# Performance work log

Measured on AMD Instinct MI355X. Metric: run time of the kernel, lower is better.

Reference implementation:

```python
import jax, jax.numpy as jnp
import numpy as np

B, L, D = 2, 1024, 2048
E, K = 8, 2
H, HS = 1408, 2816


def setup_inputs() -> dict:
    key = jax.random.key(0)
    ks = jax.random.split(key, 9)
    s = 0.02  # param init scale
    return {
        "x": jax.random.normal(ks[0], (B, L, D), dtype=jnp.float32),
        "gate_w": jax.random.normal(ks[1], (E, D), dtype=jnp.float32) * s,
        "w_gate": jax.random.normal(ks[2], (E, D, H), dtype=jnp.float32) * s,
        "w_up": jax.random.normal(ks[3], (E, D, H), dtype=jnp.float32) * s,
        "w_down": jax.random.normal(ks[4], (E, H, D), dtype=jnp.float32) * s,
        "shgate_w": jax.random.normal(ks[5], (D,), dtype=jnp.float32) * s,
        "shw_gate": jax.random.normal(ks[6], (D, HS), dtype=jnp.float32) * s,
        "shw_up": jax.random.normal(ks[7], (D, HS), dtype=jnp.float32) * s,
        "shw_down": jax.random.normal(ks[8], (HS, D), dtype=jnp.float32) * s,
    }


def reference(x, gate_w, w_gate, w_up, w_down, shgate_w, shw_gate, shw_up, shw_down):
    b, l, d = x.shape
    xf = x.reshape(-1, d)  # [T, D]

    # --- router: softmax over expert logits, top-k, renormalize ---
    logits = jnp.einsum("td,ed->te", xf.astype(jnp.float32), gate_w)
    probs = jax.nn.softmax(logits.astype(jnp.float32), axis=-1)  # [T, E]
    weights, indices = jax.lax.top_k(probs, K)                   # [T, K]
    weights = (weights / weights.sum(-1, keepdims=True)).astype(x.dtype)

    # per-token combine weight for each expert: sum of top-k weights routed to e
    onehot = jax.nn.one_hot(indices, E, dtype=x.dtype)           # [T, K, E]
    combine = jnp.einsum("tk,tke->te", weights, onehot)          # [T, E]

    # --- experts (dense vectorized equivalent of masked gather/scatter loop) ---
    g = jnp.einsum("td,edh->teh", xf, w_gate)
    u = jnp.einsum("td,edh->teh", xf, w_up)
    h = jax.nn.silu(g) * u                                       # [T, E, H]
    # fused down-proj + weighted combine; accumulate in fp32 like the original
    out = jnp.einsum("teh,ehd,te->td", h.astype(jnp.float32),
                     w_down.astype(jnp.float32), combine.astype(jnp.float32))

    # --- shared expert with sigmoid gate ---
    sgate = jax.nn.sigmoid(xf @ shgate_w)[:, None]               # [T, 1]
    sh = (jax.nn.silu(xf @ shw_gate) * (xf @ shw_up)) @ shw_down  # [T, D]
    out = out + (sgate * sh).astype(jnp.float32)

    return out.astype(x.dtype).reshape(b, l, d)
```

## Files before the change

kernel.cpp:

```cpp
#include <hip/hip_runtime.h>
#include <hip/hip_bf16.h>
#include <math.h>

#define T_TOK 2048
#define Dd    2048
#define Ee    8
#define Hh    1408
#define HSs   2816
#define CAP   1024

typedef __attribute__((ext_vector_type(8))) __bf16 bf16x8;
typedef __attribute__((ext_vector_type(4))) __bf16 bf16x4;
typedef __attribute__((ext_vector_type(4))) float  f32x4;

#define MFMA(a, b, c) __builtin_amdgcn_mfma_f32_16x16x32_bf16(a, b, c, 0, 0, 0)

__device__ __forceinline__ void async_copy16(const __bf16* g, __bf16* l) {
    __builtin_amdgcn_global_load_lds(
        (const __attribute__((address_space(1))) unsigned int*)g,
        (__attribute__((address_space(3))) unsigned int*)l, 16, 0, 0);
}

__global__ void init_cnt(int* __restrict__ cnt) {
    if (threadIdx.x < Ee) cnt[threadIdx.x] = 0;
}

__global__ __launch_bounds__(256) void router_kernel(
    const float* __restrict__ x, const float* __restrict__ gate_w,
    const float* __restrict__ shgate_w,
    int* __restrict__ cnt, int* __restrict__ ptok,
    float* __restrict__ pw, float* __restrict__ sgate)
{
    const int t = blockIdx.x;
    const int tid = threadIdx.x;
    const float* xt = x + (size_t)t * Dd;

    float acc[Ee];
#pragma unroll
    for (int e = 0; e < Ee; e++) acc[e] = 0.f;
    float accs = 0.f;

    for (int d = tid; d < Dd; d += 256) {
        float xv = xt[d];
#pragma unroll
        for (int e = 0; e < Ee; e++) acc[e] += xv * gate_w[e * Dd + d];
        accs += xv * shgate_w[d];
    }

    __shared__ float red[Ee + 1][256];
#pragma unroll
    for (int e = 0; e < Ee; e++) red[e][tid] = acc[e];
    red[Ee][tid] = accs;
    __syncthreads();

    for (int s = 128; s > 0; s >>= 1) {
        if (tid < s) {
#pragma unroll
            for (int e = 0; e <= Ee; e++) red[e][tid] += red[e][tid + s];
        }
        __syncthreads();
    }

    if (tid == 0) {
        float l0 = -1e30f, l1 = -1e30f;
        int i0 = 0, i1 = 0;
#pragma unroll
        for (int e = 0; e < Ee; e++) {
            float v = red[e][0];
            if (v > l0) { l1 = l0; i1 = i0; l0 = v; i0 = e; }
            else if (v > l1) { l1 = v; i1 = e; }
        }
        float w0 = 1.f / (1.f + expf(l1 - l0));
        float w1 = 1.f - w0;

        int p0 = atomicAdd(&cnt[i0], 1);
        if (p0 < CAP) { ptok[i0 * CAP + p0] = t; pw[i0 * CAP + p0] = w0; }
        int p1 = atomicAdd(&cnt[i1], 1);
        if (p1 < CAP) { ptok[i1 * CAP + p1] = t; pw[i1 * CAP + p1] = w1; }

        sgate[t] = 1.f / (1.f + expf(-red[Ee][0]));
    }
}

__global__ __launch_bounds__(256) void cvt_x(const float* __restrict__ src,
                                             __bf16* __restrict__ dst)
{
    int i = blockIdx.x * 256 + threadIdx.x;
    float4 v = ((const float4*)src)[i];
    bf16x4 o = { (__bf16)v.x, (__bf16)v.y, (__bf16)v.z, (__bf16)v.w };
    ((bf16x4*)dst)[i] = o;
}

__global__ __launch_bounds__(256) void transpose_cvt(
    const float* __restrict__ src, __bf16* __restrict__ dst, int R, int C)
{
    const size_t bstride = (size_t)R * C;
    src += blockIdx.z * bstride;
    dst += blockIdx.z * bstride;
    __shared__ float tile[32][33];
    const int tx = threadIdx.x, ty = threadIdx.y;
    const int c0 = blockIdx.x * 32, r0 = blockIdx.y * 32;
#pragma unroll
    for (int j = 0; j < 4; j++)
        tile[ty + 8 * j][tx] = src[(size_t)(r0 + ty + 8 * j) * C + c0 + tx];
    __syncthreads();
#pragma unroll
    for (int j = 0; j < 4; j++)
        dst[(size_t)(c0 + ty + 8 * j) * R + r0 + tx] = (__bf16)tile[tx][ty + 8 * j];
}

__global__ __launch_bounds__(256, 3) void gateup_expert(
    const __bf16* __restrict__ xb,
    const __bf16* __restrict__ wgT, const __bf16* __restrict__ wuT,
    const int* __restrict__ cnt, const int* __restrict__ ptok,
    __bf16* __restrict__ hq)
{
    const int e = blockIdx.x >> 3, mt = blockIdx.x & 7;
    int n = cnt[e]; if (n > CAP) n = CAP;
    const int m0 = mt * 128;
    if (m0 >= n) return;
    const int h0 = blockIdx.y * 64;
    const int tid = threadIdx.x, lane = tid & 63, wave = tid >> 6;

    __shared__ __align__(16) __bf16 As[128 * 32];
    __shared__ __align__(16) __bf16 Bgs[64 * 32];
    __shared__ __align__(16) __bf16 Bus[64 * 32];
    __shared__ int tok_s[128];

    if (tid < 128) {
        int i = m0 + tid; int ic = i < n ? i : n - 1;
        tok_s[tid] = ptok[e * CAP + ic];
    }
    __syncthreads();

    const int kq = (tid & 3) * 8;
    const int r1 = tid >> 2, r2 = 64 + (tid >> 2);
    const __bf16* ga1 = xb + (size_t)tok_s[r1] * Dd + kq;
    const __bf16* ga2 = xb + (size_t)tok_s[r2] * Dd + kq;
    const size_t wbase = (size_t)e * Hh * Dd + (size_t)(h0 + (tid >> 2)) * Dd + kq;
    const __bf16* gbg = wgT + wbase;
    const __bf16* gbu = wuT + wbase;
    __bf16* la1 = As + tid * 8; __bf16* la2 = As + (tid + 256) * 8;
    __bf16* lbg = Bgs + tid * 8; __bf16* lbu = Bus + tid * 8;

    f32x4 accg[2][4] = {}, accu[2][4] = {};
    const int q = lane >> 4, m = lane & 15;

    for (int k0 = 0; k0 < Dd; k0 += 32) {
        async_copy16(ga1 + k0, la1);
        async_copy16(ga2 + k0, la2);
        async_copy16(gbg + k0, lbg);
        async_copy16(gbu + k0, lbu);
        __syncthreads();
        bf16x8 af[2], bgf[4], buf_[4];
        af[0] = *(const bf16x8*)(As + (wave * 32 + m) * 32 + q * 8);
        af[1] = *(const bf16x8*)(As + (wave * 32 + 16 + m) * 32 + q * 8);
#pragma unroll
        for (int j = 0; j < 4; j++) {
            bgf[j]  = *(const bf16x8*)(Bgs + (j * 16 + m) * 32 + q * 8);
            buf_[j] = *(const bf16x8*)(Bus + (j * 16 + m) * 32 + q * 8);
        }
#pragma unroll
        for (int i = 0; i < 2; i++)
#pragma unroll
            for (int j = 0; j < 4; j++) {
                accg[i][j] = MFMA(af[i], bgf[j], accg[i][j]);
                accu[i][j] = MFMA(af[i], buf_[j], accu[i][j]);
            }
        __syncthreads();
    }

#pragma unroll
    for (int i = 0; i < 2; i++)
#pragma unroll
        for (int r = 0; r < 4; r++) {
            int row = wave * 32 + i * 16 + q * 4 + r;
            size_t p = (size_t)(e * CAP + m0 + row);
#pragma unroll
            for (int j = 0; j < 4; j++) {
                int h = h0 + j * 16 + m;
                float g = accg[i][j][r], u = accu[i][j][r];
                float s = g / (1.f + __expf(-g));
                hq[p * Hh + h] = (__bf16)(s * u);
            }
        }
}

__global__ __launch_bounds__(256, 3) void gateup_shared(
    const __bf16* __restrict__ xb,
    const __bf16* __restrict__ wgT, const __bf16* __restrict__ wuT,
    __bf16* __restrict__ shh)
{
    const int m0 = blockIdx.x * 128;
    const int h0 = blockIdx.y * 64;
    const int tid = threadIdx.x, lane = tid & 63, wave = tid >> 6;

    __shared__ __align__(16) __bf16 As[128 * 32];
    __shared__ __align__(16) __bf16 Bgs[64 * 32];
    __shared__ __align__(16) __bf16 Bus[64 * 32];

    const int kq = (tid & 3) * 8;
    const __bf16* ga1 = xb + (size_t)(m0 + (tid >> 2)) * Dd + kq;
    const __bf16* ga2 = xb + (size_t)(m0 + 64 + (tid >> 2)) * Dd + kq;
    const size_t wbase = (size_t)(h0 + (tid >> 2)) * Dd + kq;
    const __bf16* gbg = wgT + wbase;
    const __bf16* gbu = wuT + wbase;
    __bf16* la1 = As + tid * 8; __bf16* la2 = As + (tid + 256) * 8;
    __bf16* lbg = Bgs + tid * 8; __bf16* lbu = Bus + tid * 8;

    f32x4 accg[2][4] = {}, accu[2][4] = {};
    const int q = lane >> 4, m = lane & 15;

    for (int k0 = 0; k0 < Dd; k0 += 32) {
        async_copy16(ga1 + k0, la1);
        async_copy16(ga2 + k0, la2);
        async_copy16(gbg + k0, lbg);
        async_copy16(gbu + k0, lbu);
        __syncthreads();
        bf16x8 af[2], bgf[4], buf_[4];
        af[0] = *(const bf16x8*)(As + (wave * 32 + m) * 32 + q * 8);
        af[1] = *(const bf16x8*)(As + (wave * 32 + 16 + m) * 32 + q * 8);
#pragma unroll
        for (int j = 0; j < 4; j++) {
            bgf[j]  = *(const bf16x8*)(Bgs + (j * 16 + m) * 32 + q * 8);
            buf_[j] = *(const bf16x8*)(Bus + (j * 16 + m) * 32 + q * 8);
        }
#pragma unroll
        for (int i = 0; i < 2; i++)
#pragma unroll
            for (int j = 0; j < 4; j++) {
                accg[i][j] = MFMA(af[i], bgf[j], accg[i][j]);
                accu[i][j] = MFMA(af[i], buf_[j], accu[i][j]);
            }
        __syncthreads();
    }

#pragma unroll
    for (int i = 0; i < 2; i++)
#pragma unroll
        for (int r = 0; r < 4; r++) {
            int row = wave * 32 + i * 16 + q * 4 + r;
#pragma unroll
            for (int j = 0; j < 4; j++) {
                int h = h0 + j * 16 + m;
                float g = accg[i][j][r], u = accu[i][j][r];
                float s = g / (1.f + __expf(-g));
                shh[(size_t)(m0 + row) * HSs + h] = (__bf16)(s * u);
            }
        }
}

__global__ __launch_bounds__(256, 3) void down_shared(
    const __bf16* __restrict__ A,
    const __bf16* __restrict__ BT,
    const float* __restrict__ sgate,
    float* __restrict__ out)
{
    const int m0 = blockIdx.x * 128, n0 = blockIdx.y * 128;
    const int tid = threadIdx.x, lane = tid & 63, wave = tid >> 6;
    const int wr = wave >> 1, wc = wave & 1;

    __shared__ __align__(16) __bf16 As[128 * 32];
    __shared__ __align__(16) __bf16 Bs[128 * 32];

    const int kq = (tid & 3) * 8;
    const __bf16* ga1 = A + (size_t)(m0 + (tid >> 2)) * HSs + kq;
    const __bf16* ga2 = A + (size_t)(m0 + 64 + (tid >> 2)) * HSs + kq;
    const __bf16* gb1 = BT + (size_t)(n0 + (tid >> 2)) * HSs + kq;
    const __bf16* gb2 = BT + (size_t)(n0 + 64 + (tid >> 2)) * HSs + kq;
    __bf16* la1 = As + tid * 8; __bf16* la2 = As + (tid + 256) * 8;
    __bf16* lb1 = Bs + tid * 8; __bf16* lb2 = Bs + (tid + 256) * 8;

    f32x4 acc[4][4] = {};
    const int q = lane >> 4, m = lane & 15;

    for (int k0 = 0; k0 < HSs; k0 += 32) {
        async_copy16(ga1 + k0, la1);
        async_copy16(ga2 + k0, la2);
        async_copy16(gb1 + k0, lb1);
        async_copy16(gb2 + k0, lb2);
        __syncthreads();
        bf16x8 af[4], bf[4];
#pragma unroll
        for (int i = 0; i < 4; i++) {
            af[i] = *(const bf16x8*)(As + (wr * 64 + i * 16 + m) * 32 + q * 8);
            bf[i] = *(const bf16x8*)(Bs + (wc * 64 + i * 16 + m) * 32 + q * 8);
        }
#pragma unroll
        for (int i = 0; i < 4; i++)
#pragma unroll
            for (int j = 0; j < 4; j++)
                acc[i][j] = MFMA(af[i], bf[j], acc[i][j]);
        __syncthreads();
    }

#pragma unroll
    for (int i = 0; i < 4; i++)
#pragma unroll
        for (int r = 0; r < 4; r++) {
            int t = m0 + wr * 64 + i * 16 + q * 4 + r;
            float sg = sgate[t];
#pragma unroll
            for (int j = 0; j < 4; j++) {
                int d = n0 + wc * 64 + j * 16 + m;
                out[(size_t)t * Dd + d] = sg * acc[i][j][r];
            }
        }
}

__global__ __launch_bounds__(256, 3) void down_expert(
    const __bf16* __restrict__ hq,
    const __bf16* __restrict__ wdT,
    const int* __restrict__ cnt, const int* __restrict__ ptok,
    const float* __restrict__ pw,
    float* __restrict__ out)
{
    const int e = blockIdx.x >> 3, mt = blockIdx.x & 7;
    int n = cnt[e]; if (n > CAP) n = CAP;
    const int m0 = mt * 128;
    if (m0 >= n) return;
    const int n0 = blockIdx.y * 128;
    const int tid = threadIdx.x, lane = tid & 63, wave = tid >> 6;
    const int wr = wave >> 1, wc = wave & 1;

    __shared__ __align__(16) __bf16 As[128 * 32];
    __shared__ __align__(16) __bf16 Bs[128 * 32];
    __shared__ int   tok_s[128];
    __shared__ float w_s[128];

    if (tid < 128) {
        int i = m0 + tid; int ic = i < n ? i : n - 1;
        tok_s[tid] = ptok[e * CAP + ic];
        w_s[tid] = (i < n) ? pw[e * CAP + ic] : 0.f;
    }

    const int kq = (tid & 3) * 8;
    int i1 = m0 + (tid >> 2);       if (i1 > n - 1) i1 = n - 1;
    int i2 = m0 + 64 + (tid >> 2);  if (i2 > n - 1) i2 = n - 1;
    const __bf16* ga1 = hq + (size_t)(e * CAP + i1) * Hh + kq;
    const __bf16* ga2 = hq + (size_t)(e * CAP + i2) * Hh + kq;
    const __bf16* gb1 = wdT + ((size_t)e * Dd + n0 + (tid >> 2)) * Hh + kq;
    const __bf16* gb2 = wdT + ((size_t)e * Dd + n0 + 64 + (tid >> 2)) * Hh + kq;
    __bf16* la1 = As + tid * 8; __bf16* la2 = As + (tid + 256) * 8;
    __bf16* lb1 = Bs + tid * 8; __bf16* lb2 = Bs + (tid + 256) * 8;

    f32x4 acc[4][4] = {};
    const int q = lane >> 4, m = lane & 15;

    for (int k0 = 0; k0 < Hh; k0 += 32) {
        async_copy16(ga1 + k0, la1);
        async_copy16(ga2 + k0, la2);
        async_copy16(gb1 + k0, lb1);
        async_copy16(gb2 + k0, lb2);
        __syncthreads();
        bf16x8 af[4], bf[4];
#pragma unroll
        for (int i = 0; i < 4; i++) {
            af[i] = *(const bf16x8*)(As + (wr * 64 + i * 16 + m) * 32 + q * 8);
            bf[i] = *(const bf16x8*)(Bs + (wc * 64 + i * 16 + m) * 32 + q * 8);
        }
#pragma unroll
        for (int i = 0; i < 4; i++)
#pragma unroll
            for (int j = 0; j < 4; j++)
                acc[i][j] = MFMA(af[i], bf[j], acc[i][j]);
        __syncthreads();
    }

#pragma unroll
    for (int i = 0; i < 4; i++)
#pragma unroll
        for (int r = 0; r < 4; r++) {
            int row = wr * 64 + i * 16 + q * 4 + r;
            if (m0 + row < n) {
                int   tok = tok_s[row];
                float w   = w_s[row];
#pragma unroll
                for (int j = 0; j < 4; j++) {
                    int d = n0 + wc * 64 + j * 16 + m;
                    atomicAdd(&out[(size_t)tok * Dd + d], w * acc[i][j][r]);
                }
            }
        }
}

extern "C" void kernel_launch(void* const* d_in, const int* in_sizes, int n_in,
                              void* d_out, int out_size, void* d_ws, size_t ws_size,
                              hipStream_t stream) {
    const float* x        = (const float*)d_in[0];
    const float* gate_w   = (const float*)d_in[1];
    const float* w_gate   = (const float*)d_in[2];
    const float* w_up     = (const float*)d_in[3];
    const float* w_down   = (const float*)d_in[4];
    const float* shgate_w = (const float*)d_in[5];
    const float* shw_gate = (const float*)d_in[6];
    const float* shw_up   = (const float*)d_in[7];
    const float* shw_down = (const float*)d_in[8];
    float* out = (float*)d_out;

    char* ws = (char*)d_ws;
    size_t off = 0;
    auto alloc = [&](size_t bytes) { char* p = ws + off; off = (off + bytes + 255) & ~(size_t)255; return p; };
    int*    cnt    = (int*)   alloc(Ee * 4);
    int*    ptok   = (int*)   alloc(Ee * CAP * 4);
    float*  pw     = (float*) alloc(Ee * CAP * 4);
    float*  sgate  = (float*) alloc(T_TOK * 4);
    __bf16* xb     = (__bf16*)alloc((size_t)T_TOK * Dd * 2);
    __bf16* wgT    = (__bf16*)alloc((size_t)Ee * Hh * Dd * 2);
    __bf16* wuT    = (__bf16*)alloc((size_t)Ee * Hh * Dd * 2);
    __bf16* wdT    = (__bf16*)alloc((size_t)Ee * Dd * Hh * 2);
    __bf16* shwgT  = (__bf16*)alloc((size_t)HSs * Dd * 2);
    __bf16* shwuT  = (__bf16*)alloc((size_t)HSs * Dd * 2);
    __bf16* shwdT  = (__bf16*)alloc((size_t)Dd * HSs * 2);
    __bf16* hq     = (__bf16*)alloc((size_t)Ee * CAP * Hh * 2);
    __bf16* shh    = (__bf16*)alloc((size_t)T_TOK * HSs * 2);

    dim3 b256(256), bT(32, 8);

    init_cnt<<<dim3(1), dim3(64), 0, stream>>>(cnt);
    cvt_x<<<dim3(T_TOK * Dd / 4 / 256), b256, 0, stream>>>(x, xb);
    transpose_cvt<<<dim3(Hh / 32, Dd / 32, Ee), bT, 0, stream>>>(w_gate, wgT, Dd, Hh);
    transpose_cvt<<<dim3(Hh / 32, Dd / 32, Ee), bT, 0, stream>>>(w_up, wuT, Dd, Hh);
    transpose_cvt<<<dim3(Dd / 32, Hh / 32, Ee), bT, 0, stream>>>(w_down, wdT, Hh, Dd);
    transpose_cvt<<<dim3(HSs / 32, Dd / 32, 1), bT, 0, stream>>>(shw_gate, shwgT, Dd, HSs);
    transpose_cvt<<<dim3(HSs / 32, Dd / 32, 1), bT, 0, stream>>>(shw_up, shwuT, Dd, HSs);
    transpose_cvt<<<dim3(Dd / 32, HSs / 32, 1), bT, 0, stream>>>(shw_down, shwdT, HSs, Dd);

    router_kernel<<<dim3(T_TOK), b256, 0, stream>>>(x, gate_w, shgate_w, cnt, ptok, pw, sgate);

    gateup_expert<<<dim3(Ee * 8, Hh / 64), b256, 0, stream>>>(xb, wgT, wuT, cnt, ptok, hq);
    gateup_shared<<<dim3(T_TOK / 128, HSs / 64), b256, 0, stream>>>(xb, shwgT, shwuT, shh);
    down_shared<<<dim3(T_TOK / 128, Dd / 128), b256, 0, stream>>>(shh, shwdT, sgate, out);
    down_expert<<<dim3(Ee * 8, Dd / 128), b256, 0, stream>>>(hq, wdT, cnt, ptok, pw, out);
}
```

Measured before the change: 764.2 us.

## Merge shared/expert GEMMs into single launches, double-buffer LDS, replace atomics with combine

Folds the fp32-to-bf16 conversion of x into the router. The shared and expert gate/up GEMMs become one launch, and likewise the two down-projection GEMMs, so their blocks can overlap. Both GEMM kernels now double-buffer their LDS tiles to overlap the next async load with the MFMA work. Expert down-projection results go to a scratch buffer (aliased onto the gate-weight workspace) and a separate combine kernel gathers them per token with the routing weights, replacing fp32 atomicAdd scatter. The cost is doubled LDS use, which may lower occupancy, plus extra global traffic for the dexp round trip.

```diff
diff --git a/kernel.cpp b/kernel.cpp
--- a/kernel.cpp
+++ b/kernel.cpp
@@ -29,7 +29,8 @@
     const float* __restrict__ x, const float* __restrict__ gate_w,
     const float* __restrict__ shgate_w,
     int* __restrict__ cnt, int* __restrict__ ptok,
-    float* __restrict__ pw, float* __restrict__ sgate)
+    int* __restrict__ slot, float* __restrict__ swt,
+    float* __restrict__ sgate, __bf16* __restrict__ xb)
 {
     const int t = blockIdx.x;
     const int tid = threadIdx.x;
@@ -42,6 +43,7 @@
 
     for (int d = tid; d < Dd; d += 256) {
         float xv = xt[d];
+        xb[(size_t)t * Dd + d] = (__bf16)xv;
 #pragma unroll
         for (int e = 0; e < Ee; e++) acc[e] += xv * gate_w[e * Dd + d];
         accs += xv * shgate_w[d];
@@ -74,21 +76,14 @@
         float w1 = 1.f - w0;
 
         int p0 = atomicAdd(&cnt[i0], 1);
-        if (p0 < CAP) { ptok[i0 * CAP + p0] = t; pw[i0 * CAP + p0] = w0; }
+        if (p0 < CAP) { ptok[i0 * CAP + p0] = t; slot[t * 2] = i0 * CAP + p0; swt[t * 2] = w0; }
+        else          { slot[t * 2] = 0; swt[t * 2] = 0.f; }
         int p1 = atomicAdd(&cnt[i1], 1);
-        if (p1 < CAP) { ptok[i1 * CAP + p1] = t; pw[i1 * CAP + p1] = w1; }
+        if (p1 < CAP) { ptok[i1 * CAP + p1] = t; slot[t * 2 + 1] = i1 * CAP + p1; swt[t * 2 + 1] = w1; }
+        else          { slot[t * 2 + 1] = 0; swt[t * 2 + 1] = 0.f; }
 
         sgate[t] = 1.f / (1.f + expf(-red[Ee][0]));
     }
-}
-
-__global__ __launch_bounds__(256) void cvt_x(const float* __restrict__ src,
-                                             __bf16* __restrict__ dst)
-{
-    int i = blockIdx.x * 256 + threadIdx.x;
-    float4 v = ((const float4*)src)[i];
-    bf16x4 o = { (__bf16)v.x, (__bf16)v.y, (__bf16)v.z, (__bf16)v.w };
-    ((bf16x4*)dst)[i] = o;
 }
 
 __global__ __launch_bounds__(256) void transpose_cvt(
@@ -109,56 +104,77 @@
         dst[(size_t)(c0 + ty + 8 * j) * R + r0 + tx] = (__bf16)tile[tx][ty + 8 * j];
 }
 
-__global__ __launch_bounds__(256, 3) void gateup_expert(
+#define GU_SH_BLOCKS ((T_TOK / 128) * (HSs / 64))
+#define GU_EX_BLOCKS (Ee * 8 * (Hh / 64))
+
+__global__ __launch_bounds__(256, 3) void gateup_all(
     const __bf16* __restrict__ xb,
     const __bf16* __restrict__ wgT, const __bf16* __restrict__ wuT,
+    const __bf16* __restrict__ swgT, const __bf16* __restrict__ swuT,
     const int* __restrict__ cnt, const int* __restrict__ ptok,
-    __bf16* __restrict__ hq)
-{
-    const int e = blockIdx.x >> 3, mt = blockIdx.x & 7;
-    int n = cnt[e]; if (n > CAP) n = CAP;
-    const int m0 = mt * 128;
-    if (m0 >= n) return;
-    const int h0 = blockIdx.y * 64;
+    __bf16* __restrict__ hq, __bf16* __restrict__ shh)
+{
     const int tid = threadIdx.x, lane = tid & 63, wave = tid >> 6;
-
-    __shared__ __align__(16) __bf16 As[128 * 32];
-    __shared__ __align__(16) __bf16 Bgs[64 * 32];
-    __shared__ __align__(16) __bf16 Bus[64 * 32];
+    __shared__ __align__(16) __bf16 As[2][128 * 32];
+    __shared__ __align__(16) __bf16 Bg[2][64 * 32];
+    __shared__ __align__(16) __bf16 Bu[2][64 * 32];
     __shared__ int tok_s[128];
 
-    if (tid < 128) {
-        int i = m0 + tid; int ic = i < n ? i : n - 1;
-        tok_s[tid] = ptok[e * CAP + ic];
-    }
-    __syncthreads();
-
+    const int bid = blockIdx.x;
     const int kq = (tid & 3) * 8;
-    const int r1 = tid >> 2, r2 = 64 + (tid >> 2);
-    const __bf16* ga1 = xb + (size_t)tok_s[r1] * Dd + kq;
-    const __bf16* ga2 = xb + (size_t)tok_s[r2] * Dd + kq;
-    const size_t wbase = (size_t)e * Hh * Dd + (size_t)(h0 + (tid >> 2)) * Dd + kq;
-    const __bf16* gbg = wgT + wbase;
-    const __bf16* gbu = wuT + wbase;
-    __bf16* la1 = As + tid * 8; __bf16* la2 = As + (tid + 256) * 8;
-    __bf16* lbg = Bgs + tid * 8; __bf16* lbu = Bus + tid * 8;
+    const __bf16 *wg, *wu, *ga1, *ga2;
+    __bf16* outp;
+    int ostride, m0, h0;
+
+    if (bid < GU_SH_BLOCKS) {
+        int ht = bid % 44, mt = bid / 44;
+        m0 = mt * 128; h0 = ht * 64;
+        wg = swgT; wu = swuT;
+        outp = shh; ostride = HSs;
+        ga1 = xb + (size_t)(m0 + (tid >> 2)) * Dd + kq;
+        ga2 = xb + (size_t)(m0 + 64 + (tid >> 2)) * Dd + kq;
+    } else {
+        int b2 = bid - GU_SH_BLOCKS;
+        int em = b2 & 63, ht = b2 >> 6;
+        int e = em & 7, mt = em >> 3;
+        int n = cnt[e]; if (n > CAP) n = CAP;
+        m0 = mt * 128;
+        if (m0 >= n) return;
+        h0 = ht * 64;
+        wg = wgT + (size_t)e * Hh * Dd; wu = wuT + (size_t)e * Hh * Dd;
+        outp = hq + (size_t)e * CAP * Hh; ostride = Hh;
+        if (tid < 128) {
+            int i = m0 + tid; int ic = i < n ? i : n - 1;
+            tok_s[tid] = ptok[e * CAP + ic];
+        }
+        __syncthreads();
+        ga1 = xb + (size_t)tok_s[tid >> 2] * Dd + kq;
+        ga2 = xb + (size_t)tok_s[64 + (tid >> 2)] * Dd + kq;
+    }
+    const __bf16* gbg = wg + (size_t)(h0 + (tid >> 2)) * Dd + kq;
+    const __bf16* gbu = wu + (size_t)(h0 + (tid >> 2)) * Dd + kq;
 
     f32x4 accg[2][4] = {}, accu[2][4] = {};
     const int q = lane >> 4, m = lane & 15;
 
-    for (int k0 = 0; k0 < Dd; k0 += 32) {
-        async_copy16(ga1 + k0, la1);
-        async_copy16(ga2 + k0, la2);
-        async_copy16(gbg + k0, lbg);
-        async_copy16(gbu + k0, lbu);
-        __syncthreads();
+#define GU_STAGE(bb, k0) do {                              \
+    async_copy16(ga1 + (k0), As[bb] + tid * 8);            \
+    async_copy16(ga2 + (k0), As[bb] + (tid + 256) * 8);    \
+    async_copy16(gbg + (k0), Bg[bb] + tid * 8);            \
+    async_copy16(gbu + (k0), Bu[bb] + tid * 8); } while (0)
+
+    GU_STAGE(0, 0);
+    __syncthreads();
+    int cur = 0;
+    for (int t = 0; t < Dd / 32; ++t) {
+        if (t + 1 < Dd / 32) GU_STAGE(cur ^ 1, (t + 1) * 32);
         bf16x8 af[2], bgf[4], buf_[4];
-        af[0] = *(const bf16x8*)(As + (wave * 32 + m) * 32 + q * 8);
-        af[1] = *(const bf16x8*)(As + (wave * 32 + 16 + m) * 32 + q * 8);
+        af[0] = *(const bf16x8*)(As[cur] + (wave * 32 + m) * 32 + q * 8);
+        af[1] = *(const bf16x8*)(As[cur] + (wave * 32 + 16 + m) * 32 + q * 8);
 #pragma unroll
         for (int j = 0; j < 4; j++) {
-            bgf[j]  = *(const bf16x8*)(Bgs + (j * 16 + m) * 32 + q * 8);
-            buf_[j] = *(const bf16x8*)(Bus + (j * 16 + m) * 32 + q * 8);
+            bgf[j]  = *(const bf16x8*)(Bg[cur] + (j * 16 + m) * 32 + q * 8);
+            buf_[j] = *(const bf16x8*)(Bu[cur] + (j * 16 + m) * 32 + q * 8);
         }
 #pragma unroll
         for (int i = 0; i < 2; i++)
@@ -168,123 +184,87 @@
                 accu[i][j] = MFMA(af[i], buf_[j], accu[i][j]);
             }
         __syncthreads();
-    }
+        cur ^= 1;
+    }
+#undef GU_STAGE
 
 #pragma unroll
     for (int i = 0; i < 2; i++)
 #pragma unroll
         for (int r = 0; r < 4; r++) {
-            int row = wave * 32 + i * 16 + q * 4 + r;
-            size_t p = (size_t)(e * CAP + m0 + row);
+            int row = m0 + wave * 32 + i * 16 + q * 4 + r;
 #pragma unroll
             for (int j = 0; j < 4; j++) {
                 int h = h0 + j * 16 + m;
                 float g = accg[i][j][r], u = accu[i][j][r];
                 float s = g / (1.f + __expf(-g));
-                hq[p * Hh + h] = (__bf16)(s * u);
+                outp[(size_t)row * ostride + h] = (__bf16)(s * u);
             }
         }
 }
 
-__global__ __launch_bounds__(256, 3) void gateup_shared(
-    const __bf16* __restrict__ xb,
-    const __bf16* __restrict__ wgT, const __bf16* __restrict__ wuT,
-    __bf16* __restrict__ shh)
-{
-    const int m0 = blockIdx.x * 128;
-    const int h0 = blockIdx.y * 64;
-    const int tid = threadIdx.x, lane = tid & 63, wave = tid >> 6;
-
-    __shared__ __align__(16) __bf16 As[128 * 32];
-    __shared__ __align__(16) __bf16 Bgs[64 * 32];
-    __shared__ __align__(16) __bf16 Bus[64 * 32];
-
-    const int kq = (tid & 3) * 8;
-    const __bf16* ga1 = xb + (size_t)(m0 + (tid >> 2)) * Dd + kq;
-    const __bf16* ga2 = xb + (size_t)(m0 + 64 + (tid >> 2)) * Dd + kq;
-    const size_t wbase = (size_t)(h0 + (tid >> 2)) * Dd + kq;
-    const __bf16* gbg = wgT + wbase;
-    const __bf16* gbu = wuT + wbase;
-    __bf16* la1 = As + tid * 8; __bf16* la2 = As + (tid + 256) * 8;
-    __bf16* lbg = Bgs + tid * 8; __bf16* lbu = Bus + tid * 8;
-
-    f32x4 accg[2][4] = {}, accu[2][4] = {};
-    const int q = lane >> 4, m = lane & 15;
-
-    for (int k0 = 0; k0 < Dd; k0 += 32) {
-        async_copy16(ga1 + k0, la1);
-        async_copy16(ga2 + k0, la2);
-        async_copy16(gbg + k0, lbg);
-        async_copy16(gbu + k0, lbu);
-        __syncthreads();
-        bf16x8 af[2], bgf[4], buf_[4];
-        af[0] = *(const bf16x8*)(As + (wave * 32 + m) * 32 + q * 8);
-        af[1] = *(const bf16x8*)(As + (wave * 32 + 16 + m) * 32 + q * 8);
-#pragma unroll
-        for (int j = 0; j < 4; j++) {
-            bgf[j]  = *(const bf16x8*)(Bgs + (j * 16 + m) * 32 + q * 8);
-            buf_[j] = *(const bf16x8*)(Bus + (j * 16 + m) * 32 + q * 8);
-        }
-#pragma unroll
-        for (int i = 0; i < 2; i++)
-#pragma unroll
-            for (int j = 0; j < 4; j++) {
-                accg[i][j] = MFMA(af[i], bgf[j], accg[i][j]);
-                accu[i][j] = MFMA(af[i], buf_[j], accu[i][j]);
-            }
-        __syncthreads();
-    }
-
-#pragma unroll
-    for (int i = 0; i < 2; i++)
-#pragma unroll
-        for (int r = 0; r < 4; r++) {
-            int row = wave * 32 + i * 16 + q * 4 + r;
-#pragma unroll
-            for (int j = 0; j < 4; j++) {
-                int h = h0 + j * 16 + m;
-                float g = accg[i][j][r], u = accu[i][j][r];
-                float s = g / (1.f + __expf(-g));
-                shh[(size_t)(m0 + row) * HSs + h] = (__bf16)(s * u);
-            }
-        }
-}
-
-__global__ __launch_bounds__(256, 3) void down_shared(
-    const __bf16* __restrict__ A,
-    const __bf16* __restrict__ BT,
-    const float* __restrict__ sgate,
-    float* __restrict__ out)
-{
-    const int m0 = blockIdx.x * 128, n0 = blockIdx.y * 128;
+#define DN_SH_BLOCKS ((T_TOK / 128) * (Dd / 128))
+#define DN_EX_BLOCKS (Ee * 8 * (Dd / 128))
+
+__global__ __launch_bounds__(256, 3) void down_all(
+    const __bf16* __restrict__ shh, const __bf16* __restrict__ shwdT,
+    const __bf16* __restrict__ hq, const __bf16* __restrict__ wdT,
+    const int* __restrict__ cnt, const float* __restrict__ sgate,
+    float* __restrict__ out, float* __restrict__ dexp)
+{
     const int tid = threadIdx.x, lane = tid & 63, wave = tid >> 6;
     const int wr = wave >> 1, wc = wave & 1;
-
-    __shared__ __align__(16) __bf16 As[128 * 32];
-    __shared__ __align__(16) __bf16 Bs[128 * 32];
+    __shared__ __align__(16) __bf16 As[2][128 * 32];
+    __shared__ __align__(16) __bf16 Bs[2][128 * 32];
+
+    const int bid = blockIdx.x;
+    const __bf16 *A, *BT;
+    int m0, n0, K, shared_path, arow_base = 0;
+
+    if (bid < DN_SH_BLOCKS) {
+        int nt = bid & 15, mt = bid >> 4;
+        m0 = mt * 128; n0 = nt * 128; K = HSs;
+        A = shh; BT = shwdT; shared_path = 1;
+    } else {
+        int b2 = bid - DN_SH_BLOCKS;
+        int em = b2 & 63, nt = b2 >> 6;
+        int e = em & 7, mt = em >> 3;
+        int n = cnt[e]; if (n > CAP) n = CAP;
+        m0 = mt * 128;
+        if (m0 >= n) return;
+        n0 = nt * 128; K = Hh;
+        A = hq + (size_t)e * CAP * Hh;
+        BT = wdT + (size_t)e * Dd * Hh;
+        arow_base = e * CAP;
+        shared_path = 0;
+    }
 
     const int kq = (tid & 3) * 8;
-    const __bf16* ga1 = A + (size_t)(m0 + (tid >> 2)) * HSs + kq;
-    const __bf16* ga2 = A + (size_t)(m0 + 64 + (tid >> 2)) * HSs + kq;
-    const __bf16* gb1 = BT + (size_t)(n0 + (tid >> 2)) * HSs + kq;
-    const __bf16* gb2 = BT + (size_t)(n0 + 64 + (tid >> 2)) * HSs + kq;
-    __bf16* la1 = As + tid * 8; __bf16* la2 = As + (tid + 256) * 8;
-    __bf16* lb1 = Bs + tid * 8; __bf16* lb2 = Bs + (tid + 256) * 8;
+    const __bf16* ga1 = A + (size_t)(m0 + (tid >> 2)) * K + kq;
+    const __bf16* ga2 = A + (size_t)(m0 + 64 + (tid >> 2)) * K + kq;
+    const __bf16* gb1 = BT + (size_t)(n0 + (tid >> 2)) * K + kq;
+    const __bf16* gb2 = BT + (size_t)(n0 + 64 + (tid >> 2)) * K + kq;
 
     f32x4 acc[4][4] = {};
     const int q = lane >> 4, m = lane & 15;
 
-    for (int k0 = 0; k0 < HSs; k0 += 32) {
-        async_copy16(ga1 + k0, la1);
-        async_copy16(ga2 + k0, la2);
-        async_copy16(gb1 + k0, lb1);
-        async_copy16(gb2 + k0, lb2);
-        __syncthreads();
+#define DN_STAGE(bb, k0) do {                              \
+    async_copy16(ga1 + (k0), As[bb] + tid * 8);            \
+    async_copy16(ga2 + (k0), As[bb] + (tid + 256) * 8);    \
+    async_copy16(gb1 + (k0), Bs[bb] + tid * 8);            \
+    async_copy16(gb2 + (k0), Bs[bb] + (tid + 256) * 8); } while (0)
+
+    DN_STAGE(0, 0);
+    __syncthreads();
+    int cur = 0;
+    const int ntk = K / 32;
+    for (int t = 0; t < ntk; ++t) {
+        if (t + 1 < ntk) DN_STAGE(cur ^ 1, (t + 1) * 32);
         bf16x8 af[4], bf[4];
 #pragma unroll
         for (int i = 0; i < 4; i++) {
-            af[i] = *(const bf16x8*)(As + (wr * 64 + i * 16 + m) * 32 + q * 8);
-            bf[i] = *(const bf16x8*)(Bs + (wc * 64 + i * 16 + m) * 32 + q * 8);
+            af[i] = *(const bf16x8*)(As[cur] + (wr * 64 + i * 16 + m) * 32 + q * 8);
+            bf[i] = *(const bf16x8*)(Bs[cur] + (wc * 64 + i * 16 + m) * 32 + q * 8);
         }
 #pragma unroll
         for (int i = 0; i < 4; i++)
@@ -292,96 +272,54 @@
             for (int j = 0; j < 4; j++)
                 acc[i][j] = MFMA(af[i], bf[j], acc[i][j]);
         __syncthreads();
-    }
-
-#pragma unroll
-    for (int i = 0; i < 4; i++)
-#pragma unroll
-        for (int r = 0; r < 4; r++) {
-            int t = m0 + wr * 64 + i * 16 + q * 4 + r;
-            float sg = sgate[t];
-#pragma unroll
-            for (int j = 0; j < 4; j++) {
-                int d = n0 + wc * 64 + j * 16 + m;
-                out[(size_t)t * Dd + d] = sg * acc[i][j][r];
+        cur ^= 1;
+    }
+#undef DN_STAGE
+
+    if (shared_path) {
+#pragma unroll
+        for (int i = 0; i < 4; i++)
+#pragma unroll
+            for (int r = 0; r < 4; r++) {
+                int trow = m0 + wr * 64 + i * 16 + q * 4 + r;
+                float sg = sgate[trow];
+#pragma unroll
+                for (int j = 0; j < 4; j++)
+                    out[(size_t)trow * Dd + n0 + wc * 64 + j * 16 + m] = sg * acc[i][j][r];
             }
-        }
-}
-
-__global__ __launch_bounds__(256, 3) void down_expert(
-    const __bf16* __restrict__ hq,
-    const __bf16* __restrict__ wdT,
-    const int* __restrict__ cnt, const int* __restrict__ ptok,
-    const float* __restrict__ pw,
-    float* __restrict__ out)
-{
-    const int e = blockIdx.x >> 3, mt = blockIdx.x & 7;
-    int n = cnt[e]; if (n > CAP) n = CAP;
-    const int m0 = mt * 128;
-    if (m0 >= n) return;
-    const int n0 = blockIdx.y * 128;
-    const int tid = threadIdx.x, lane = tid & 63, wave = tid >> 6;
-    const int wr = wave >> 1, wc = wave & 1;
-
-    __shared__ __align__(16) __bf16 As[128 * 32];
-    __shared__ __align__(16) __bf16 Bs[128 * 32];
-    __shared__ int   tok_s[128];
-    __shared__ float w_s[128];
-
-    if (tid < 128) {
-        int i = m0 + tid; int ic = i < n ? i : n - 1;
-        tok_s[tid] = ptok[e * CAP + ic];
-        w_s[tid] = (i < n) ? pw[e * CAP + ic] : 0.f;
-    }
-
-    const int kq = (tid & 3) * 8;
-    int i1 = m0 + (tid >> 2);       if (i1 > n - 1) i1 = n - 1;
-    int i2 = m0 + 64 + (tid >> 2);  if (i2 > n - 1) i2 = n - 1;
-    const __bf16* ga1 = hq + (size_t)(e * CAP + i1) * Hh + kq;
-    const __bf16* ga2 = hq + (size_t)(e * CAP + i2) * Hh + kq;
-    const __bf16* gb1 = wdT + ((size_t)e * Dd + n0 + (tid >> 2)) * Hh + kq;
-    const __bf16* gb2 = wdT + ((size_t)e * Dd + n0 + 64 + (tid >> 2)) * Hh + kq;
-    __bf16* la1 = As + tid * 8; __bf16* la2 = As + (tid + 256) * 8;
-    __bf16* lb1 = Bs + tid * 8; __bf16* lb2 = Bs + (tid + 256) * 8;
-
-    f32x4 acc[4][4] = {};
-    const int q = lane >> 4, m = lane & 15;
-
-    for (int k0 = 0; k0 < Hh; k0 += 32) {
-        async_copy16(ga1 + k0, la1);
-        async_copy16(ga2 + k0, la2);
-        async_copy16(gb1 + k0, lb1);
-        async_copy16(gb2 + k0, lb2);
-        __syncthreads();
-        bf16x8 af[4], bf[4];
-#pragma unroll
-        for (int i = 0; i < 4; i++) {
-            af[i] = *(const bf16x8*)(As + (wr * 64 + i * 16 + m) * 32 + q * 8);
-            bf[i] = *(const bf16x8*)(Bs + (wc * 64 + i * 16 + m) * 32 + q * 8);
-        }
+    } else {
 #pragma unroll
         for (int i = 0; i < 4; i++)
 #pragma unroll
-            for (int j = 0; j < 4; j++)
-                acc[i][j] = MFMA(af[i], bf[j], acc[i][j]);
-        __syncthreads();
-    }
-
-#pragma unroll
-    for (int i = 0; i < 4; i++)
-#pragma unroll
-        for (int r = 0; r < 4; r++) {
-            int row = wr * 64 + i * 16 + q * 4 + r;
-            if (m0 + row < n) {
-                int   tok = tok_s[row];
-                float w   = w_s[row];
-#pragma unroll
-                for (int j = 0; j < 4; j++) {
-                    int d = n0 + wc * 64 + j * 16 + m;
-                    atomicAdd(&out[(size_t)tok * Dd + d], w * acc[i][j][r]);
-                }
+            for (int r = 0; r < 4; r++) {
+                int row = arow_base + m0 + wr * 64 + i * 16 + q * 4 + r;
+#pragma unroll
+                for (int j = 0; j < 4; j++)
+                    dexp[(size_t)row * Dd + n0 + wc * 64 + j * 16 + m] = acc[i][j][r];
             }
-        }
+    }
+}
+
+__global__ __launch_bounds__(256) void combine_kernel(
+    const float* __restrict__ dexp, const int* __restrict__ slot,
+    const float* __restrict__ swt, float* __restrict__ out)
+{
+    const int t = blockIdx.x, tid = threadIdx.x;
+    const int s0 = slot[t * 2], s1 = slot[t * 2 + 1];
+    const float w0 = swt[t * 2], w1 = swt[t * 2 + 1];
+    const float4* d0 = (const float4*)(dexp + (size_t)s0 * Dd);
+    const float4* d1 = (const float4*)(dexp + (size_t)s1 * Dd);
+    float4* o = (float4*)(out + (size_t)t * Dd);
+#pragma unroll
+    for (int it = 0; it < 2; ++it) {
+        int i = tid + it * 256;
+        float4 a = o[i], b0 = d0[i], b1 = d1[i];
+        a.x += w0 * b0.x + w1 * b1.x;
+        a.y += w0 * b0.y + w1 * b1.y;
+        a.z += w0 * b0.z + w1 * b1.z;
+        a.w += w0 * b0.w + w1 * b1.w;
+        o[i] = a;
+    }
 }
 
 extern "C" void kernel_launch(void* const* d_in, const int* in_sizes, int n_in,
@@ -403,7 +341,8 @@
     auto alloc = [&](size_t bytes) { char* p = ws + off; off = (off + bytes + 255) & ~(size_t)255; return p; };
     int*    cnt    = (int*)   alloc(Ee * 4);
     int*    ptok   = (int*)   alloc(Ee * CAP * 4);
-    float*  pw     = (float*) alloc(Ee * CAP * 4);
+    int*    slot   = (int*)   alloc(T_TOK * 2 * 4);
+    float*  swt    = (float*) alloc(T_TOK * 2 * 4);
     float*  sgate  = (float*) alloc(T_TOK * 4);
     __bf16* xb     = (__bf16*)alloc((size_t)T_TOK * Dd * 2);
     __bf16* wgT    = (__bf16*)alloc((size_t)Ee * Hh * Dd * 2);
@@ -414,11 +353,11 @@
     __bf16* shwdT  = (__bf16*)alloc((size_t)Dd * HSs * 2);
     __bf16* hq     = (__bf16*)alloc((size_t)Ee * CAP * Hh * 2);
     __bf16* shh    = (__bf16*)alloc((size_t)T_TOK * HSs * 2);
+    float* dexp = (float*)wgT;
 
     dim3 b256(256), bT(32, 8);
 
     init_cnt<<<dim3(1), dim3(64), 0, stream>>>(cnt);
-    cvt_x<<<dim3(T_TOK * Dd / 4 / 256), b256, 0, stream>>>(x, xb);
     transpose_cvt<<<dim3(Hh / 32, Dd / 32, Ee), bT, 0, stream>>>(w_gate, wgT, Dd, Hh);
     transpose_cvt<<<dim3(Hh / 32, Dd / 32, Ee), bT, 0, stream>>>(w_up, wuT, Dd, Hh);
     transpose_cvt<<<dim3(Dd / 32, Hh / 32, Ee), bT, 0, stream>>>(w_down, wdT, Hh, Dd);
@@ -426,10 +365,14 @@
     transpose_cvt<<<dim3(HSs / 32, Dd / 32, 1), bT, 0, stream>>>(shw_up, shwuT, Dd, HSs);
     transpose_cvt<<<dim3(Dd / 32, HSs / 32, 1), bT, 0, stream>>>(shw_down, shwdT, HSs, Dd);
 
-    router_kernel<<<dim3(T_TOK), b256, 0, stream>>>(x, gate_w, shgate_w, cnt, ptok, pw, sgate);
-
-    gateup_expert<<<dim3(Ee * 8, Hh / 64), b256, 0, stream>>>(xb, wgT, wuT, cnt, ptok, hq);
-    gateup_shared<<<dim3(T_TOK / 128, HSs / 64), b256, 0, stream>>>(xb, shwgT, shwuT, shh);
-    down_shared<<<dim3(T_TOK / 128, Dd / 128), b256, 0, stream>>>(shh, shwdT, sgate, out);
-    down_expert<<<dim3(Ee * 8, Dd / 128), b256, 0, stream>>>(hq, wdT, cnt, ptok, pw, out);
-}
+    router_kernel<<<dim3(T_TOK), b256, 0, stream>>>(x, gate_w, shgate_w,
+                                                    cnt, ptok, slot, swt, sgate, xb);
+
+    gateup_all<<<dim3(GU_SH_BLOCKS + GU_EX_BLOCKS), b256, 0, stream>>>(
+        xb, wgT, wuT, shwgT, shwuT, cnt, ptok, hq, shh);
+
+    down_all<<<dim3(DN_SH_BLOCKS + DN_EX_BLOCKS), b256, 0, stream>>>(
+        shh, shwdT, hq, wdT, cnt, sgate, out, dexp);
+
+    combine_kernel<<<dim3(T_TOK), b256, 0, stream>>>(dexp, slot, swt, out);
+}
```

Result: faster. 686.8 us (-10.1%).
